# Kernel optimization log

Measured on AMD Instinct MI355X. Metric: run time of the kernel, lower is better.

The kernel has to match this reference:

```python
import jax, jax.numpy as jnp
import numpy as np

ALPHA = 0.2   # LeakyReLU negative slope
BN_EPS = 1e-5
NEG_INF = -9e15  # same masking constant as the torch source


def make_quaternion_mul(kernel):
    # kernel: [in_features//4, out_features]; returns hamilton [in_features, out_features]
    r, i, j, k = jnp.split(kernel, 4, axis=1)
    r2 = jnp.concatenate([r, -i, -j, -k], axis=1)
    i2 = jnp.concatenate([i,  r, -k,  j], axis=1)
    j2 = jnp.concatenate([j,  k,  r, -i], axis=1)
    k2 = jnp.concatenate([k, -j,  i,  r], axis=1)
    return jnp.concatenate([r2, i2, j2, k2], axis=0)


def setup_inputs() -> dict:
    key = jax.random.key(0)
    k1, k2, k3, k4 = jax.random.split(key, 4)
    N, IN_F, OUT_F = 8192, 1024, 256
    inp = jax.random.normal(k1, (N, IN_F), dtype=jnp.float32)
    adj = jax.random.randint(k2, (N, N), 0, 2, dtype=jnp.int32)
    # xavier-uniform-like init scales
    W = jax.random.uniform(k3, (IN_F // 4, OUT_F), dtype=jnp.float32,
                           minval=-1.0, maxval=1.0) * np.sqrt(6.0 / (IN_F // 4 + OUT_F))
    a = jax.random.uniform(k4, (2 * OUT_F, 1), dtype=jnp.float32,
                           minval=-1.0, maxval=1.0) * np.sqrt(6.0 / (2 * OUT_F + 1))
    gamma = jnp.ones((OUT_F,), dtype=jnp.float32)
    beta = jnp.zeros((OUT_F,), dtype=jnp.float32)
    return {"input": inp, "adj": adj, "W": W, "a": a, "gamma": gamma, "beta": beta}


def reference(input, adj, W, a, gamma, beta):
    hamilton = make_quaternion_mul(W)            # [IN_F, OUT_F]
    h = input @ hamilton                         # [N, OUT_F]
    F_out = h.shape[1]
    # e[i, j] = leakyrelu(concat(h_i, h_j) . a) = leakyrelu(h_i.a1 + h_j.a2)
    a1 = a[:F_out, 0]
    a2 = a[F_out:, 0]
    e = jax.nn.leaky_relu((h @ a1)[:, None] + (h @ a2)[None, :],
                          negative_slope=ALPHA)  # [N, N]
    e = jnp.where(adj > 0, e, NEG_INF)
    attention = jax.nn.softmax(e, axis=1)        # masked softmax over neighbors
    h_prime = attention @ h                      # [N, OUT_F]
    # BatchNorm1d (training mode: batch statistics, biased variance)
    mean = jnp.mean(h_prime, axis=0)
    var = jnp.var(h_prime, axis=0)
    h_norm = (h_prime - mean) * jax.lax.rsqrt(var + BN_EPS) * gamma + beta
    return jax.nn.elu(h_norm)                    # concat=True -> elu
```

## Files before the change

### kernel.cpp

```cpp
#include <hip/hip_runtime.h>
#include <stdint.h>

#define ALPHA 0.2f
#define LOG2E 1.4426950408889634f

typedef __attribute__((ext_vector_type(8))) short short8;
typedef __attribute__((ext_vector_type(4))) float f32x4;
typedef __attribute__((ext_vector_type(16))) float f32x16;
typedef __attribute__((ext_vector_type(4))) int int4v;
typedef __attribute__((ext_vector_type(2))) unsigned int uint2v;

#if __has_builtin(__builtin_amdgcn_exp2f)
#define EXP2(x) __builtin_amdgcn_exp2f(x)
#else
#define EXP2(x) exp2f(x)
#endif

__device__ __forceinline__ unsigned short f2bf(float x){
  union { float f; uint32_t u; } v; v.f = x;
  uint32_t u = v.u;
  u += 0x7FFFu + ((u >> 16) & 1u);
  return (unsigned short)(u >> 16);
}
__device__ __forceinline__ float bf2f(unsigned short s){
  union { uint32_t u; float f; } v; v.u = ((uint32_t)s) << 16; return v.f;
}
__device__ __forceinline__ unsigned encf(float x){
  unsigned u = __float_as_uint(x);
  return (u & 0x80000000u) ? ~u : (u | 0x80000000u);
}
__device__ __forceinline__ float decf(unsigned u){
  return (u & 0x80000000u) ? __uint_as_float(u & 0x7FFFFFFFu) : __uint_as_float(~u);
}

__global__ void k_ham(const float* __restrict__ W, unsigned short* __restrict__ hi,
                      unsigned short* __restrict__ lo, unsigned* __restrict__ S2enc,
                      float* __restrict__ gsum, float* __restrict__ gsumsq){
  if (blockIdx.x == 0){
    if (threadIdx.x == 0) S2enc[0] = 0u;
    gsum[threadIdx.x] = 0.f; gsumsq[threadIdx.x] = 0.f;
  }
  int id = blockIdx.x * 256 + threadIdx.x;
  int c = id >> 10, k = id & 1023;
  int b = k >> 8, r = k & 255;
  int cb = c >> 6, col = c & 63;
  const int   comp[4][4] = {{0,1,2,3},{1,0,3,2},{2,3,0,1},{3,2,1,0}};
  const float sgn [4][4] = {{1.f,-1.f,-1.f,-1.f},{1.f,1.f,-1.f,1.f},
                            {1.f,1.f,1.f,-1.f},{1.f,-1.f,1.f,1.f}};
  float v = sgn[b][cb] * W[r * 256 + comp[b][cb] * 64 + col];
  unsigned short h = f2bf(v);
  hi[id] = h;
  lo[id] = f2bf(v - bf2f(h));
}

__global__ __launch_bounds__(256) void k_work(
    const float* __restrict__ inp, const int* __restrict__ adj,
    const unsigned short* __restrict__ hamHi, const unsigned short* __restrict__ hamLo,
    const float* __restrict__ avec, unsigned short* __restrict__ hT,
    float* __restrict__ s1s, float* __restrict__ s2s, unsigned* __restrict__ S2enc,
    unsigned long long* __restrict__ bm){
  if (blockIdx.x >= 256){
    const int lane = threadIdx.x & 63;
    const size_t wid = ((size_t)(blockIdx.x - 256) * 256 + threadIdx.x) >> 6;
    const size_t W0 = wid * 1024;
    unsigned long long b[16];
#pragma unroll
    for (int q = 0; q < 4; ++q){
      int4v a = *(const int4v*)(adj + W0 + 256*q + 4*lane);
#pragma unroll
      for (int k = 0; k < 4; ++k) b[4*q + k] = __ballot(a[k] > 0);
    }
    if (lane < 16){
      unsigned long long v = b[0];
#pragma unroll
      for (int m = 1; m < 16; ++m) v = (lane == m) ? b[m] : v;
      bm[W0/64 + lane] = v;
    }
    return;
  }
  int i0 = blockIdx.x * 32;
  int w = threadIdx.x >> 6, lane = threadIdx.x & 63;
  int mi = lane & 15, g = lane >> 4;
  int cbase = w * 64;
  f32x4 acc[2][4];
#pragma unroll
  for (int mf=0; mf<2; ++mf)
#pragma unroll
    for (int nf=0; nf<4; ++nf) acc[mf][nf] = (f32x4){0.f,0.f,0.f,0.f};

  for (int k0 = 0; k0 < 1024; k0 += 32){
    short8 ah[2], al[2];
#pragma unroll
    for (int mf=0; mf<2; ++mf){
      const float* ap = inp + (size_t)(i0 + 16*mf + mi) * 1024 + k0 + 8*g;
      f32x4 x0 = *(const f32x4*)ap;
      f32x4 x1 = *(const f32x4*)(ap + 4);
#pragma unroll
      for (int e=0; e<8; ++e){
        float x = (e < 4) ? x0[e] : x1[e-4];
        unsigned short h = f2bf(x);
        ah[mf][e] = (short)h;
        al[mf][e] = (short)f2bf(x - bf2f(h));
      }
    }
    short8 bh[4], bl[4];
#pragma unroll
    for (int nf=0; nf<4; ++nf){
      size_t off = (size_t)(cbase + 16*nf + mi) * 1024 + k0 + 8*g;
      bh[nf] = *(const short8*)(hamHi + off);
      bl[nf] = *(const short8*)(hamLo + off);
    }
#pragma unroll
    for (int mf=0; mf<2; ++mf)
#pragma unroll
      for (int nf=0; nf<4; ++nf){
        acc[mf][nf] = __builtin_amdgcn_mfma_f32_16x16x32_bf16(ah[mf], bh[nf], acc[mf][nf], 0,0,0);
        acc[mf][nf] = __builtin_amdgcn_mfma_f32_16x16x32_bf16(ah[mf], bl[nf], acc[mf][nf], 0,0,0);
        acc[mf][nf] = __builtin_amdgcn_mfma_f32_16x16x32_bf16(al[mf], bh[nf], acc[mf][nf], 0,0,0);
      }
  }
  float p1[2][4] = {{0,0,0,0},{0,0,0,0}}, p2[2][4] = {{0,0,0,0},{0,0,0,0}};
#pragma unroll
  for (int nf=0; nf<4; ++nf){
    int c = cbase + 16*nf + mi;
    float a1c = avec[c], a2c = avec[256 + c];
    int Sc = (c & 7) << 3;
#pragma unroll
    for (int mf=0; mf<2; ++mf){
      int ibase = i0 + 16*mf + 4*g;
      uint2v u;
      u[0] = (uint32_t)f2bf(acc[mf][nf][0]) | ((uint32_t)f2bf(acc[mf][nf][1]) << 16);
      u[1] = (uint32_t)f2bf(acc[mf][nf][2]) | ((uint32_t)f2bf(acc[mf][nf][3]) << 16);
      *(uint2v*)(hT + (size_t)c * 8192 + (size_t)(ibase ^ Sc)) = u;
#pragma unroll
      for (int rg=0; rg<4; ++rg){
        p1[mf][rg] += acc[mf][nf][rg] * a1c;
        p2[mf][rg] += acc[mf][nf][rg] * a2c;
      }
    }
  }
#pragma unroll
  for (int off=1; off<16; off<<=1){
#pragma unroll
    for (int mf=0; mf<2; ++mf)
#pragma unroll
      for (int rg=0; rg<4; ++rg){
        p1[mf][rg] += __shfl_xor(p1[mf][rg], off);
        p2[mf][rg] += __shfl_xor(p2[mf][rg], off);
      }
  }
  __shared__ float red1[4][32], red2[4][32];
  if (mi == 0){
#pragma unroll
    for (int mf=0; mf<2; ++mf)
#pragma unroll
      for (int rg=0; rg<4; ++rg){
        red1[w][16*mf + 4*g + rg] = p1[mf][rg];
        red2[w][16*mf + 4*g + rg] = p2[mf][rg];
      }
  }
  __syncthreads();
  if (threadIdx.x < 32){
    int r = threadIdx.x;
    float v1 = red1[0][r] + red1[1][r] + red1[2][r] + red1[3][r];
    float v2 = red2[0][r] + red2[1][r] + red2[2][r] + red2[3][r];
    s1s[i0 + r] = v1 * LOG2E;
    float v2s = v2 * LOG2E;
    s2s[i0 + r] = v2s;
    float m = v2s;
#pragma unroll
    for (int off=1; off<32; off<<=1) m = fmaxf(m, __shfl_xor(m, off));
    if (r == 0) atomicMax(S2enc, encf(m));
  }
}

#define STAGE(t, b) do { \
    _Pragma("unroll") \
    for (int r_ = 0; r_ < 8; ++r_){ \
      int ch_ = tid + r_*256; \
      const unsigned short* gp_ = hT + (size_t)(ch_ >> 3)*8192 + jw0 + (t)*64 + (ch_&7)*8; \
      __builtin_amdgcn_global_load_lds((const __attribute__((address_space(1))) void*)(const void*)gp_, \
          (__attribute__((address_space(3))) void*)(void*)&hbuf[(b)][ch_*8], 16, 0, 0); \
    } } while(0)

__global__ __launch_bounds__(256,1) void k_attn(
    const unsigned long long* __restrict__ bm, const unsigned short* __restrict__ hT,
    const float* __restrict__ s1s, const float* __restrict__ s2s,
    const unsigned* __restrict__ S2enc, float* __restrict__ accp, float* __restrict__ Zp){
  __shared__ unsigned short hbuf[2][256*64];
  __shared__ float s2l[2048];
  const int tid = threadIdx.x;
  const int id = blockIdx.x;
  const int js = (id & 7) >> 1;
  const int rb = ((id >> 3) << 1) | (id & 1);
  const int w = tid >> 6, lane = tid & 63;
  const int r31 = lane & 31, hi = lane >> 5;
  const int i0w = rb * 128 + w * 32;
  const int jw0 = js * 2048;

  { f32x4 v0 = *(const f32x4*)(s2s + jw0 + tid*8);
    f32x4 v1 = *(const f32x4*)(s2s + jw0 + tid*8 + 4);
    *(f32x4*)&s2l[tid*8] = v0; *(f32x4*)&s2l[tid*8 + 4] = v1; }

  const float S2MAX = decf(S2enc[0]);
  const float s1v = s1s[i0w + r31];
  const float xm = s1v + S2MAX;
  const float m2 = fmaxf(xm, ALPHA * xm);
  const float P1 = s1v - m2;
  const float P2 = ALPHA * s1v - m2;

  const unsigned long long* brow = bm + (size_t)(i0w + r31) * 128 + js * 32;

  f32x16 acc[8];
#pragma unroll
  for (int nf=0; nf<8; ++nf)
#pragma unroll
    for (int q=0; q<16; ++q) acc[nf][q] = 0.f;
  float zac = 0.f;

  unsigned long long Wc[4], Wn[4];
#pragma unroll
  for (int k=0;k<4;++k) Wc[k] = brow[k];
  STAGE(0, 0);
  __syncthreads();

  for (int tile = 0; tile < 32; ++tile){
    const int buf = tile & 1;
    if ((tile & 3) == 0){
      if (tile){
#pragma unroll
        for (int k=0;k<4;++k) Wc[k] = Wn[k];
      }
      if (tile + 4 < 32){
        const unsigned long long* p = brow + (tile >> 2)*4 + 4;
#pragma unroll
        for (int k=0;k<4;++k) Wn[k] = p[k];
      }
    }
    if (tile < 31) STAGE(tile + 1, buf ^ 1);
#pragma unroll
    for (int ks=0; ks<4; ++ks){
      f32x4 sa = *(const f32x4*)&s2l[tile*64 + ks*16 + hi*8];
      f32x4 sb = *(const f32x4*)&s2l[tile*64 + ks*16 + hi*8 + 4];
      const int sh0 = ((tile & 3) << 4) + (ks << 2) + (hi << 1);
      unsigned tt[4];
#pragma unroll
      for (int k=0;k<4;++k) tt[k] = (unsigned)(Wc[k] >> sh0);
      short8 pa;
#pragma unroll
      for (int e=0; e<8; ++e){
        float s2e = (e < 4) ? sa[e] : sb[e-4];
        float t1 = P1 + s2e;
        float t2 = fmaf(ALPHA, s2e, P2);
        float pe = EXP2(fmaxf(t1, t2));
        pe = ((tt[e & 3] >> (e >> 2)) & 1u) ? pe : 0.f;
        zac += pe;
        pa[e] = (short)f2bf(pe);
      }
      const int xk = ks*16 + hi*8;
#pragma unroll
      for (int nf=0; nf<8; ++nf){
        const int c = 32*nf + r31;
        short8 b = *(const short8*)&hbuf[buf][c*64 + (xk ^ ((c&7)<<3))];
        acc[nf] = __builtin_amdgcn_mfma_f32_32x32x16_bf16(pa, b, acc[nf], 0,0,0);
      }
    }
    __syncthreads();
  }
  zac += __shfl_xor(zac, 32);
  if (lane < 32) Zp[js*8192 + i0w + lane] = zac;
#pragma unroll
  for (int nf=0; nf<8; ++nf){
    const int c = 32*nf + r31;
#pragma unroll
    for (int reg=0; reg<16; ++reg){
      const int roff = (reg&3) + 8*(reg>>2) + 4*hi;
      accp[(size_t)(js*8192 + i0w + roff)*256 + c] = acc[nf][reg];
    }
  }
}

__global__ void k_stats(const float* __restrict__ accp, const float* __restrict__ Zp,
                        float* __restrict__ hp, float* __restrict__ gsum,
                        float* __restrict__ gsumsq){
  int c = threadIdx.x;
  int r0 = blockIdx.x * 32;
  float s = 0.f, sq = 0.f;
  for (int r=0; r<32; ++r){
    int i = r0 + r;
    float z = Zp[i] + Zp[8192 + i] + Zp[16384 + i] + Zp[24576 + i];
    float inv = (z > 0.f) ? 1.f / z : 0.f;
    size_t o = (size_t)i * 256 + c;
    float v = (accp[o] + accp[o + 8192*256] + accp[o + 2*8192*256] + accp[o + 3*8192*256]) * inv;
    hp[o] = v;
    s += v; sq += v*v;
  }
  atomicAdd(&gsum[c], s);
  atomicAdd(&gsumsq[c], sq);
}

__global__ void k_bnelu(float* __restrict__ out, const float* __restrict__ gsum,
                        const float* __restrict__ gsumsq, const float* __restrict__ gamma,
                        const float* __restrict__ beta){
  int id = blockIdx.x * 256 + threadIdx.x;
  int c = id & 255;
  float mean = gsum[c] * (1.f/8192.f);
  float var  = gsumsq[c] * (1.f/8192.f) - mean*mean;
  float x = (out[id] - mean) * rsqrtf(var + 1e-5f) * gamma[c] + beta[c];
  out[id] = x > 0.f ? x : (EXP2(x * LOG2E) - 1.f);
}

extern "C" void kernel_launch(void* const* d_in, const int* in_sizes, int n_in,
                              void* d_out, int out_size, void* d_ws, size_t ws_size,
                              hipStream_t stream){
  const float* inp   = (const float*)d_in[0];
  const int*   adj   = (const int*)d_in[1];
  const float* W     = (const float*)d_in[2];
  const float* avec  = (const float*)d_in[3];
  const float* gamma = (const float*)d_in[4];
  const float* beta  = (const float*)d_in[5];
  float* out = (float*)d_out;

  char* ws = (char*)d_ws;
  float* accp = (float*)ws;
  float* Zp   = accp + 4*8192*256;
  unsigned short* hamHi = (unsigned short*)(Zp + 32768);
  unsigned short* hamLo = hamHi + 262144;
  unsigned short* hT    = hamLo + 262144;
  float* s1s = (float*)(hT + 2097152);
  float* s2s = s1s + 8192;
  unsigned* S2enc = (unsigned*)(s2s + 8192);
  float* gsum   = (float*)(S2enc + 64);
  float* gsumsq = gsum + 256;
  unsigned long long* bm = (unsigned long long*)(gsumsq + 256);

  k_ham<<<1024, 256, 0, stream>>>(W, hamHi, hamLo, S2enc, gsum, gsumsq);
  k_work<<<16640, 256, 0, stream>>>(inp, adj, hamHi, hamLo, avec, hT, s1s, s2s, S2enc, bm);
  k_attn<<<256, 256, 0, stream>>>(bm, hT, s1s, s2s, S2enc, accp, Zp);
  k_stats<<<256, 256, 0, stream>>>(accp, Zp, out, gsum, gsumsq);
  k_bnelu<<<8192, 256, 0, stream>>>(out, gsum, gsumsq, gamma, beta);
}
```

Before: 177.3 us.

## Split attention over 8 column slices with tiled h layout and packed bf16 convert

The attention kernel now splits the neighbour dimension into 8 slices instead of 4 and launches 512 blocks, with launch bounds allowing two blocks per CU. The h matrix is stored in a tiled layout of 8-column groups, so each stage is one contiguous copy and the LDS read no longer needs the XOR swizzle. Probabilities are converted to bf16 with a packed hardware instruction. The cost is twice the partial-sum traffic (8 partial accumulators written and then reduced in k_stats), plus possible LDS bank conflicts from the unswizzled reads.

```diff
diff --git a/kernel.cpp b/kernel.cpp
--- a/kernel.cpp
+++ b/kernel.cpp
@@ -24,6 +24,11 @@
 }
 __device__ __forceinline__ float bf2f(unsigned short s){
   union { uint32_t u; float f; } v; v.u = ((uint32_t)s) << 16; return v.f;
+}
+__device__ __forceinline__ unsigned cvt_pk_bf16(float lo, float hi){
+  unsigned r;
+  asm("v_cvt_pk_bf16_f32 %0, %1, %2" : "=v"(r) : "v"(lo), "v"(hi));
+  return r;
 }
 __device__ __forceinline__ unsigned encf(float x){
   unsigned u = __float_as_uint(x);
@@ -56,7 +61,7 @@
 __global__ __launch_bounds__(256) void k_work(
     const float* __restrict__ inp, const int* __restrict__ adj,
     const unsigned short* __restrict__ hamHi, const unsigned short* __restrict__ hamLo,
-    const float* __restrict__ avec, unsigned short* __restrict__ hT,
+    const float* __restrict__ avec, unsigned short* __restrict__ hTt,
     float* __restrict__ s1s, float* __restrict__ s2s, unsigned* __restrict__ S2enc,
     unsigned long long* __restrict__ bm){
   if (blockIdx.x >= 256){
@@ -124,14 +129,13 @@
   for (int nf=0; nf<4; ++nf){
     int c = cbase + 16*nf + mi;
     float a1c = avec[c], a2c = avec[256 + c];
-    int Sc = (c & 7) << 3;
 #pragma unroll
     for (int mf=0; mf<2; ++mf){
-      int ibase = i0 + 16*mf + 4*g;
+      int jg = (i0 + 16*mf + 4*g) >> 3;
       uint2v u;
       u[0] = (uint32_t)f2bf(acc[mf][nf][0]) | ((uint32_t)f2bf(acc[mf][nf][1]) << 16);
       u[1] = (uint32_t)f2bf(acc[mf][nf][2]) | ((uint32_t)f2bf(acc[mf][nf][3]) << 16);
-      *(uint2v*)(hT + (size_t)c * 8192 + (size_t)(ibase ^ Sc)) = u;
+      *(uint2v*)(hTt + (size_t)jg * 2048 + c * 8 + (g & 1) * 4) = u;
 #pragma unroll
       for (int rg=0; rg<4; ++rg){
         p1[mf][rg] += acc[mf][nf][rg] * a1c;
@@ -175,32 +179,30 @@
 }
 
 #define STAGE(t, b) do { \
+    const unsigned short* sp_ = hTt + (size_t)jw0 * 256 + (size_t)(t) * 16384; \
     _Pragma("unroll") \
     for (int r_ = 0; r_ < 8; ++r_){ \
       int ch_ = tid + r_*256; \
-      const unsigned short* gp_ = hT + (size_t)(ch_ >> 3)*8192 + jw0 + (t)*64 + (ch_&7)*8; \
-      __builtin_amdgcn_global_load_lds((const __attribute__((address_space(1))) void*)(const void*)gp_, \
+      __builtin_amdgcn_global_load_lds((const __attribute__((address_space(1))) void*)(const void*)(sp_ + ch_*8), \
           (__attribute__((address_space(3))) void*)(void*)&hbuf[(b)][ch_*8], 16, 0, 0); \
     } } while(0)
 
-__global__ __launch_bounds__(256,1) void k_attn(
-    const unsigned long long* __restrict__ bm, const unsigned short* __restrict__ hT,
+__global__ __launch_bounds__(256,2) void k_attn(
+    const unsigned long long* __restrict__ bm, const unsigned short* __restrict__ hTt,
     const float* __restrict__ s1s, const float* __restrict__ s2s,
     const unsigned* __restrict__ S2enc, float* __restrict__ accp, float* __restrict__ Zp){
   __shared__ unsigned short hbuf[2][256*64];
-  __shared__ float s2l[2048];
+  __shared__ float s2l[1024];
   const int tid = threadIdx.x;
   const int id = blockIdx.x;
-  const int js = (id & 7) >> 1;
-  const int rb = ((id >> 3) << 1) | (id & 1);
+  const int js = id & 7;
+  const int rb = id >> 3;
   const int w = tid >> 6, lane = tid & 63;
   const int r31 = lane & 31, hi = lane >> 5;
   const int i0w = rb * 128 + w * 32;
-  const int jw0 = js * 2048;
-
-  { f32x4 v0 = *(const f32x4*)(s2s + jw0 + tid*8);
-    f32x4 v1 = *(const f32x4*)(s2s + jw0 + tid*8 + 4);
-    *(f32x4*)&s2l[tid*8] = v0; *(f32x4*)&s2l[tid*8 + 4] = v1; }
+  const int jw0 = js * 1024;
+
+  { f32x4 v = *(const f32x4*)(s2s + jw0 + tid*4); *(f32x4*)&s2l[tid*4] = v; }
 
   const float S2MAX = decf(S2enc[0]);
   const float s1v = s1s[i0w + r31];
@@ -209,7 +211,7 @@
   const float P1 = s1v - m2;
   const float P2 = ALPHA * s1v - m2;
 
-  const unsigned long long* brow = bm + (size_t)(i0w + r31) * 128 + js * 32;
+  const unsigned long long* brow = bm + (size_t)(i0w + r31) * 128 + js * 16;
 
   f32x16 acc[8];
 #pragma unroll
@@ -224,20 +226,20 @@
   STAGE(0, 0);
   __syncthreads();
 
-  for (int tile = 0; tile < 32; ++tile){
+  for (int tile = 0; tile < 16; ++tile){
     const int buf = tile & 1;
     if ((tile & 3) == 0){
       if (tile){
 #pragma unroll
         for (int k=0;k<4;++k) Wc[k] = Wn[k];
       }
-      if (tile + 4 < 32){
+      if (tile + 4 < 16){
         const unsigned long long* p = brow + (tile >> 2)*4 + 4;
 #pragma unroll
         for (int k=0;k<4;++k) Wn[k] = p[k];
       }
     }
-    if (tile < 31) STAGE(tile + 1, buf ^ 1);
+    if (tile < 15) STAGE(tile + 1, buf ^ 1);
 #pragma unroll
     for (int ks=0; ks<4; ++ks){
       f32x4 sa = *(const f32x4*)&s2l[tile*64 + ks*16 + hi*8];
@@ -246,23 +248,25 @@
       unsigned tt[4];
 #pragma unroll
       for (int k=0;k<4;++k) tt[k] = (unsigned)(Wc[k] >> sh0);
-      short8 pa;
+      float pe[8];
 #pragma unroll
       for (int e=0; e<8; ++e){
         float s2e = (e < 4) ? sa[e] : sb[e-4];
         float t1 = P1 + s2e;
         float t2 = fmaf(ALPHA, s2e, P2);
-        float pe = EXP2(fmaxf(t1, t2));
-        pe = ((tt[e & 3] >> (e >> 2)) & 1u) ? pe : 0.f;
-        zac += pe;
-        pa[e] = (short)f2bf(pe);
-      }
-      const int xk = ks*16 + hi*8;
+        float p = EXP2(fmaxf(t1, t2));
+        p = ((tt[e & 3] >> (e >> 2)) & 1u) ? p : 0.f;
+        zac += p;
+        pe[e] = p;
+      }
+      union { short8 s; unsigned u[4]; } pa;
+#pragma unroll
+      for (int wd=0; wd<4; ++wd) pa.u[wd] = cvt_pk_bf16(pe[2*wd], pe[2*wd+1]);
+      const int jbase = (2*ks + hi) * 2048;
 #pragma unroll
       for (int nf=0; nf<8; ++nf){
-        const int c = 32*nf + r31;
-        short8 b = *(const short8*)&hbuf[buf][c*64 + (xk ^ ((c&7)<<3))];
-        acc[nf] = __builtin_amdgcn_mfma_f32_32x32x16_bf16(pa, b, acc[nf], 0,0,0);
+        short8 b = *(const short8*)&hbuf[buf][jbase + (32*nf + r31)*8];
+        acc[nf] = __builtin_amdgcn_mfma_f32_32x32x16_bf16(pa.s, b, acc[nf], 0,0,0);
       }
     }
     __syncthreads();
@@ -288,10 +292,15 @@
   float s = 0.f, sq = 0.f;
   for (int r=0; r<32; ++r){
     int i = r0 + r;
-    float z = Zp[i] + Zp[8192 + i] + Zp[16384 + i] + Zp[24576 + i];
+    float z = 0.f;
+#pragma unroll
+    for (int s8=0; s8<8; ++s8) z += Zp[s8*8192 + i];
     float inv = (z > 0.f) ? 1.f / z : 0.f;
     size_t o = (size_t)i * 256 + c;
-    float v = (accp[o] + accp[o + 8192*256] + accp[o + 2*8192*256] + accp[o + 3*8192*256]) * inv;
+    float v = 0.f;
+#pragma unroll
+    for (int s8=0; s8<8; ++s8) v += accp[o + (size_t)s8*8192*256];
+    v *= inv;
     hp[o] = v;
     s += v; sq += v*v;
   }
@@ -323,11 +332,11 @@
 
   char* ws = (char*)d_ws;
   float* accp = (float*)ws;
-  float* Zp   = accp + 4*8192*256;
-  unsigned short* hamHi = (unsigned short*)(Zp + 32768);
+  float* Zp   = accp + (size_t)8*8192*256;
+  unsigned short* hamHi = (unsigned short*)(Zp + 65536);
   unsigned short* hamLo = hamHi + 262144;
-  unsigned short* hT    = hamLo + 262144;
-  float* s1s = (float*)(hT + 2097152);
+  unsigned short* hTt   = hamLo + 262144;
+  float* s1s = (float*)(hTt + 2097152);
   float* s2s = s1s + 8192;
   unsigned* S2enc = (unsigned*)(s2s + 8192);
   float* gsum   = (float*)(S2enc + 64);
@@ -335,8 +344,8 @@
   unsigned long long* bm = (unsigned long long*)(gsumsq + 256);
 
   k_ham<<<1024, 256, 0, stream>>>(W, hamHi, hamLo, S2enc, gsum, gsumsq);
-  k_work<<<16640, 256, 0, stream>>>(inp, adj, hamHi, hamLo, avec, hT, s1s, s2s, S2enc, bm);
-  k_attn<<<256, 256, 0, stream>>>(bm, hT, s1s, s2s, S2enc, accp, Zp);
+  k_work<<<16640, 256, 0, stream>>>(inp, adj, hamHi, hamLo, avec, hTt, s1s, s2s, S2enc, bm);
+  k_attn<<<512, 256, 0, stream>>>(bm, hTt, s1s, s2s, S2enc, accp, Zp);
   k_stats<<<256, 256, 0, stream>>>(accp, Zp, out, gsum, gsumsq);
   k_bnelu<<<8192, 256, 0, stream>>>(out, gsum, gsumsq, gamma, beta);
 }
```

After: 168.0 us. -5.2%, faster.
